# Performance work log

Measured on AMD Instinct MI355X. Metric: run time of the kernel, lower is better.

The kernel has to match this reference:

```python
import jax, jax.numpy as jnp
import numpy as np

B, S, M, KD, VD, QD, H, NQ = 256, 200, 32, 128, 256, 128, 64, 10000
TA, TB, TC = 0.075, 0.088, 1.0  # triangular membership params a, b, c


def setup_inputs() -> dict:
    key = jax.random.key(0)
    ks = jax.random.split(key, 12)
    q_data = jax.random.randint(ks[0], (B, S), 0, NQ + 1)
    # kaiming-normal-ish embedding table; padding_idx=0 row zeroed
    q_embed_weight = jax.random.normal(ks[1], (NQ + 1, QD)) * np.sqrt(2.0 / QD)
    q_embed_weight = q_embed_weight.at[0].set(0.0)
    key_mem = jax.random.normal(ks[2], (M, KD)) * np.sqrt(2.0 / KD)
    value_mem = jax.random.normal(ks[3], (M, VD)) * np.sqrt(2.0 / VD)
    in_dim = VD + QD
    s = 1.0 / np.sqrt(H)
    W_ih = jax.random.uniform(ks[4], (4 * H, in_dim), minval=-s, maxval=s)
    W_hh = jax.random.uniform(ks[5], (4 * H, H), minval=-s, maxval=s)
    b_ih = jax.random.uniform(ks[6], (4 * H,), minval=-s, maxval=s)
    b_hh = jax.random.uniform(ks[7], (4 * H,), minval=-s, maxval=s)
    W_pred = jax.random.normal(ks[8], (1, H)) * np.sqrt(2.0 / H)
    b_pred = jnp.zeros((1,))
    init_h = jax.random.normal(ks[9], (B, H))
    init_c = jax.random.normal(ks[10], (B, H))
    return dict(q_data=q_data, q_embed_weight=q_embed_weight, key_mem=key_mem,
                value_mem=value_mem, W_ih=W_ih, W_hh=W_hh, b_ih=b_ih, b_hh=b_hh,
                W_pred=W_pred, b_pred=b_pred, init_h=init_h, init_c=init_c)


def triangular_layer(cw):
    """cw: [N, M] correlation weights -> [N] unique-row indices.
    Faithful to torch: trit-quantize each weight {0,1,2}, then map each row to its
    index in the (lexicographically sorted) unique-row table, which is exactly what
    the pairwise squared-distance matmul + (dist==0).nonzero() trick computes."""
    w = jnp.minimum((cw - TA) / (TB - TA), (TC - cw) / (TC - TB))
    w = jnp.maximum(w, 0.0)
    iv = jnp.where(w >= 0.6, 2, jnp.where(w >= 0.1, 1, 0)).astype(jnp.int32)  # [N, M]
    # pack 32 trits into two int32 keys (3^16 < 2^31)
    p = jnp.power(3, jnp.arange(16, dtype=jnp.int32))  # [16]
    kh = (iv[:, :16] * p).sum(1)
    kl = (iv[:, 16:] * p).sum(1)
    order = jnp.lexsort((kl, kh))  # primary key kh
    kh_s, kl_s = kh[order], kl[order]
    change = jnp.concatenate([jnp.zeros((1,), jnp.int32),
                              ((kh_s[1:] != kh_s[:-1]) | (kl_s[1:] != kl_s[:-1])).astype(jnp.int32)])
    rank_sorted = jnp.cumsum(change)
    inv = jnp.zeros(cw.shape[0], jnp.int32).at[order].set(rank_sorted)
    return inv


def reference(q_data, q_embed_weight, key_mem, value_mem, W_ih, W_hh, b_ih, b_hh,
              W_pred, b_pred, init_h, init_c):
    q_emb = q_embed_weight[q_data]                                  # [B,S,QD]
    cw = jax.nn.softmax(jnp.einsum('bsd,md->bsm', q_emb, key_mem))  # DKVMN attention
    read = jnp.einsum('bsm,mv->bsv', cw, value_mem)                 # [B,S,VD]
    ids = triangular_layer(cw.reshape(B * S, M))                    # [B*S]
    x = jnp.concatenate([read, q_emb], axis=-1)                     # [B,S,VD+QD]

    def step(carry, xt):
        h, c = carry
        g = xt @ W_ih.T + h @ W_hh.T + b_ih + b_hh
        i, f, gg, o = jnp.split(g, 4, axis=-1)
        c = jax.nn.sigmoid(f) * c + jax.nn.sigmoid(i) * jnp.tanh(gg)
        h = jax.nn.sigmoid(o) * jnp.tanh(c)
        return (h, c), h

    _, hs = jax.lax.scan(step, (init_h, init_c), jnp.swapaxes(x, 0, 1))
    hs = jnp.swapaxes(hs, 0, 1)                                     # [B,S,H]
    pred = jax.nn.sigmoid(hs @ W_pred.T + b_pred)[..., 0]           # [B,S]
    return pred, ids
```

## Files before the change

### kernel.cpp

```cpp
#include <hip/hip_runtime.h>

#define BB 256
#define SS 200
#define MM 32
#define KDIM 128
#define VDIM 256
#define QDIM 128
#define HH 64
#define NROWS 10001
#define NSAMP (BB*SS)
#define INDIM (VDIM+QDIM)
#define DHS 8192
#define DHMASK (DHS-1)
#define XR 16
#define NB_ATTN 1251

typedef unsigned long long u64;
typedef unsigned int u32;
typedef float f16v __attribute__((ext_vector_type(16)));

__device__ __forceinline__ float fexp(float x){ return __builtin_amdgcn_exp2f(x * 1.44269504f); }
__device__ __forceinline__ float fsigm(float x){ return __builtin_amdgcn_rcpf(1.f + fexp(-x)); }
__device__ __forceinline__ float ftanh(float x){ return 1.f - 2.f*__builtin_amdgcn_rcpf(1.f + fexp(2.f*x)); }
__device__ __forceinline__ int clampq(int q){ return q < 0 ? 0 : (q > NROWS-1 ? NROWS-1 : q); }

__device__ __forceinline__ u32 hash64(u64 x){
  x ^= x >> 33; x *= 0xff51afd7ed558ccdULL;
  x ^= x >> 33; x *= 0xc4ceb9fe1a85ec53ULL;
  x ^= x >> 33;
  return (u32)x;
}

__device__ __forceinline__ u64 shflx64(u64 v, int m){
  int lo = __shfl_xor((int)(u32)v, m, 64);
  int hi = __shfl_xor((int)(u32)(v >> 32), m, 64);
  return ((u64)(u32)hi << 32) | (u32)lo;
}

__global__ void k_tr(const float* __restrict__ W_ih, const float* __restrict__ key_mem,
                     float* __restrict__ WQT4, float* __restrict__ KT,
                     float* __restrict__ WVT, u32* __restrict__ present){
  int idx = blockIdx.x*256 + threadIdx.x;
  if (idx < 131072) {
    int dd = idx & 3, j = (idx >> 2) & 255, d4 = idx >> 10;
    WQT4[idx] = W_ih[j*INDIM + VDIM + 4*d4 + dd];
  } else if (idx < 135168) {
    int t = idx - 131072;
    int m = t & 31, d = t >> 5; KT[t] = key_mem[m*KDIM + d];
  } else if (idx < 200704) {
    int t = idx - 135168;
    int j = t & 255, v = t >> 8; WVT[v*256 + j] = W_ih[j*INDIM + v];
  } else {
    int t = idx - 200704;
    if (t < NROWS) present[t] = 0u;
  }
}

__global__ __launch_bounds__(256) void k_front(
    const float* __restrict__ emb, const float* __restrict__ KT,
    const float* __restrict__ val, const float* __restrict__ WVT,
    const int* __restrict__ q_data,
    float* __restrict__ CW, u64* __restrict__ KEYT,
    float* __restrict__ VW, u32* __restrict__ present){
  int bid = blockIdx.x;
  if (bid < NB_ATTN) {
    int w = threadIdx.x >> 6, l = threadIdx.x & 63;
    int half = l >> 5, m = l & 31;
    int row = 2*w + half;
    int n = bid*8 + row;
    __shared__ float se[8][QDIM];
    {
      int rA = bid*8 + 2*w, rB = rA + 1;
      if (rA < NROWS) { se[2*w  ][l] = emb[rA*QDIM + l]; se[2*w  ][l+64] = emb[rA*QDIM + l + 64]; }
      if (rB < NROWS) { se[2*w+1][l] = emb[rB*QDIM + l]; se[2*w+1][l+64] = emb[rB*QDIM + l + 64]; }
    }
    __syncthreads();
    bool valid = (n < NROWS);
    float logit = 0.f;
    if (valid)
      for (int d = 0; d < KDIM; ++d) logit += se[row][d] * KT[d*32 + m];
    float mx = logit;
    #pragma unroll
    for (int msk = 16; msk >= 1; msk >>= 1) mx = fmaxf(mx, __shfl_xor(mx, msk, 64));
    float e = valid ? expf(logit - mx) : 0.f;
    float sum = e;
    #pragma unroll
    for (int msk = 16; msk >= 1; msk >>= 1) sum += __shfl_xor(sum, msk, 64);
    float cw = e / sum;
    float wv = fminf((cw - 0.075f)/0.013f, (1.0f - cw)/0.912f);
    wv = fmaxf(wv, 0.f);
    int iv = (wv >= 0.6f) ? 2 : ((wv >= 0.1f) ? 1 : 0);
    int ee = (m < 16) ? m + 16 : m - 16;
    u64 p3 = 1, bb = 3;
    #pragma unroll
    for (int bit = 0; bit < 5; ++bit) {
      if (ee & (1 << bit)) p3 *= bb;
      bb *= bb;
    }
    u64 term = valid ? (u64)iv * p3 : 0ULL;
    #pragma unroll
    for (int msk = 16; msk >= 1; msk >>= 1) term += shflx64(term, msk);
    if (valid) CW[n*256 + m] = cw;
    if (valid && m == 0) KEYT[n] = term;
  } else if (bid < NB_ATTN + MM) {
    int m = bid - NB_ATTN, j = threadIdx.x;
    __shared__ float sval[VDIM];
    sval[j] = val[m*VDIM + j];
    __syncthreads();
    float a0=0.f, a1=0.f, a2=0.f, a3=0.f;
    for (int v = 0; v < VDIM; v += 4) {
      a0 += sval[v+0]*WVT[(v+0)*256 + j];
      a1 += sval[v+1]*WVT[(v+1)*256 + j];
      a2 += sval[v+2]*WVT[(v+2)*256 + j];
      a3 += sval[v+3]*WVT[(v+3)*256 + j];
    }
    VW[m*256 + j] = (a0+a1)+(a2+a3);
  } else {
    int i = (bid - NB_ATTN - MM)*256 + threadIdx.x;
    if (i < NSAMP) present[clampq(q_data[i])] = 1u;
  }
}

__global__ __launch_bounds__(256) void k_xw(
    const float* __restrict__ CW, const float* __restrict__ emb,
    const float* __restrict__ VW, const float* __restrict__ WQT4,
    const float* __restrict__ b_ih, const float* __restrict__ b_hh,
    float* __restrict__ XW4){
  int base = blockIdx.x * XR;
  int j = threadIdx.x;
  __shared__ float scw[XR][32];
  __shared__ __align__(16) float ses[XR][QDIM];
  for (int idx = j; idx < XR*32; idx += 256) {
    int r = idx >> 5, m = idx & 31, n = base + r;
    scw[r][m] = (n < NROWS) ? CW[n*256 + m] : 0.f;
  }
  for (int idx = j; idx < XR*QDIM; idx += 256) {
    int r = idx >> 7, d = idx & 127, n = base + r;
    ses[r][d] = (n < NROWS) ? emb[n*QDIM + d] : 0.f;
  }
  __syncthreads();
  float bias = b_ih[j] + b_hh[j];
  float acc[XR];
  #pragma unroll
  for (int r = 0; r < XR; ++r) acc[r] = bias;
  for (int m = 0; m < MM; ++m) {
    float wv = VW[m*256 + j];
    #pragma unroll
    for (int r = 0; r < XR; ++r) acc[r] += scw[r][m] * wv;
  }
  for (int d4 = 0; d4 < QDIM/4; ++d4) {
    float4 wq = *(const float4*)(WQT4 + d4*1024 + j*4);
    #pragma unroll
    for (int r = 0; r < XR; ++r) {
      float4 ev = *(const float4*)(&ses[r][4*d4]);
      acc[r] += ev.x*wq.x + ev.y*wq.y + ev.z*wq.z + ev.w*wq.w;
    }
  }
  int gate = j >> 6, unit = j & 63;
  #pragma unroll
  for (int r = 0; r < XR; ++r)
    if (base + r < NROWS) XW4[(size_t)(base + r)*256 + 4*unit + gate] = acc[r];
}

__global__ __launch_bounds__(1024) void k_dedup(
    const u32* __restrict__ present, const u64* __restrict__ KEYT,
    u32* __restrict__ g_htab, u32* __restrict__ g_pay,
    u32* __restrict__ counter, u64* __restrict__ uniq){
  __shared__ u32 sh_tab[DHS];
  __shared__ u32 sh_pay[DHS];
  __shared__ u32 sh_cnt;
  int tid = threadIdx.x;
  for (int i = tid; i < DHS; i += 1024) sh_tab[i] = 0u;
  if (tid == 0) sh_cnt = 0u;
  __syncthreads();
  for (int n = tid; n < NROWS; n += 1024) {
    if (present[n] != 1u) continue;
    u64 key = KEYT[n];
    u32 h = hash64(key) & DHMASK;
    while (true) {
      u32 cur = sh_tab[h];
      if (cur != 0u) {
        if (KEYT[cur-1u] == key) break;
        h = (h + 1) & DHMASK; continue;
      }
      u32 prev = atomicCAS(&sh_tab[h], 0u, (u32)(n + 1));
      if (prev == 0u) {
        u32 idx = atomicAdd(&sh_cnt, 1u);
        uniq[idx] = key;
        sh_pay[h] = idx;
        break;
      }
      if (KEYT[prev-1u] == key) break;
      h = (h + 1) & DHMASK;
    }
  }
  __syncthreads();
  for (int i = tid; i < DHS; i += 1024) {
    u32 v = sh_tab[i];
    g_htab[i] = v;
    g_pay[i]  = v ? sh_pay[i] : 0u;
  }
  if (tid == 0) *counter = sh_cnt;
}

__global__ __launch_bounds__(64) void k_rank(const u64* __restrict__ uniq,
                                             const u32* __restrict__ counter,
                                             u32* __restrict__ RANK){
  u32 U = *counter;
  int u = blockIdx.x*64 + threadIdx.x;
  if (u >= (int)U) return;
  u64 mykey = uniq[u];
  u32 cnt = 0;
  for (u32 j = 0; j < U; ++j) {
    u64 k = uniq[j];
    cnt += (k < mykey) ? 1u : 0u;
  }
  RANK[u] = cnt;
}

__global__ void k_qrank(const u32* __restrict__ present, const u64* __restrict__ KEYT,
                        const u32* __restrict__ g_htab, const u32* __restrict__ g_pay,
                        const u32* __restrict__ RANK, u32* __restrict__ RANKQ){
  int n = blockIdx.x*blockDim.x + threadIdx.x;
  if (n >= NROWS || present[n] != 1u) return;
  u64 key = KEYT[n];
  u32 h = hash64(key) & DHMASK;
  while (true) {
    u32 cur = g_htab[h];
    if (cur != 0u && KEYT[cur-1u] == key) { RANKQ[n] = RANK[g_pay[h]]; return; }
    h = (h + 1) & DHMASK;
  }
}

__global__ void k_ids(const int* __restrict__ q_data, const u32* __restrict__ RANKQ,
                      float* __restrict__ out_ids){
  int i = blockIdx.x*blockDim.x + threadIdx.x;
  if (i >= NSAMP) return;
  out_ids[i] = (float)RANKQ[clampq(q_data[i])];
}

#define DOT16(acc, W, H) do { \
  acc += (W)[0]*(H)[0];   acc += (W)[1]*(H)[1];   acc += (W)[2]*(H)[2];   acc += (W)[3]*(H)[3]; \
  acc += (W)[4]*(H)[4];   acc += (W)[5]*(H)[5];   acc += (W)[6]*(H)[6];   acc += (W)[7]*(H)[7]; \
  acc += (W)[8]*(H)[8];   acc += (W)[9]*(H)[9];   acc += (W)[10]*(H)[10]; acc += (W)[11]*(H)[11]; \
  acc += (W)[12]*(H)[12]; acc += (W)[13]*(H)[13]; acc += (W)[14]*(H)[14]; acc += (W)[15]*(H)[15]; \
} while(0)

__global__ __launch_bounds__(256, 1) void k_lstm(
    const int* __restrict__ q_data, const float* __restrict__ XW4,
    const float* __restrict__ W_hh,
    const float* __restrict__ W_pred, const float* __restrict__ b_pred,
    const float* __restrict__ init_h, const float* __restrict__ init_c,
    float* __restrict__ out_pred){
  const int b = blockIdx.x;
  const int t = threadIdx.x;
  const int w = t >> 6, l = t & 63;
  const int uo = l & 15, k = l >> 4;
  const int u = 16*w + uo;
  __shared__ __align__(64) float Hbuf[SS][64];
  __shared__ int   sq[SS];
  __shared__ float swp[HH];

  for (int s = t; s < SS; s += 256) sq[s] = clampq(q_data[b*SS + s]);
  if (t < HH) swp[t] = W_pred[t];

  const float* wb = W_hh + (size_t)u*HH + 16*k;
  f16v Wi = *(const f16v*)(wb +     0);
  f16v Wf = *(const f16v*)(wb +  4096);
  f16v Wg = *(const f16v*)(wb +  8192);
  f16v Wo = *(const f16v*)(wb + 12288);

  f16v H = *(const f16v*)(init_h + (size_t)b*HH + 16*k);
  float c  = init_c[b*HH + u];
  float bp = b_pred[0];
  __syncthreads();

  float4 xwA = *(const float4*)(XW4 + (size_t)sq[0]*256 + 4*u);
  float4 xwB = *(const float4*)(XW4 + (size_t)sq[1]*256 + 4*u);

  for (int s = 0; s < SS; ++s) {
    int sp = (s + 2 < SS) ? s + 2 : SS - 1;
    float4 xwC = *(const float4*)(XW4 + (size_t)sq[sp]*256 + 4*u);
    float pi=0.f, pf=0.f, pg=0.f, po=0.f;
    DOT16(pi, Wi, H); DOT16(pf, Wf, H); DOT16(pg, Wg, H); DOT16(po, Wo, H);
    pi += __shfl_xor(pi, 16, 64); pf += __shfl_xor(pf, 16, 64);
    pg += __shfl_xor(pg, 16, 64); po += __shfl_xor(po, 16, 64);
    pi += __shfl_xor(pi, 32, 64); pf += __shfl_xor(pf, 32, 64);
    pg += __shfl_xor(pg, 32, 64); po += __shfl_xor(po, 32, 64);
    float ai = xwA.x + pi;
    float af = xwA.y + pf;
    float ag = xwA.z + pg;
    float ao = xwA.w + po;
    c = fsigm(af)*c + fsigm(ai)*ftanh(ag);
    float hh = fsigm(ao)*ftanh(c);
    if (l < 16) Hbuf[s][u] = hh;
    __syncthreads();
    H = *(const f16v*)(&Hbuf[s][16*k]);
    xwA = xwB; xwB = xwC;
  }
  __syncthreads();

  for (int s = t; s < SS; s += 256) {
    float acc = 0.f;
    #pragma unroll 16
    for (int kk = 0; kk < HH; ++kk) {
      int k2 = (kk + t) & 63;
      acc += Hbuf[s][k2] * swp[k2];
    }
    out_pred[b*SS + s] = fsigm(acc + bp);
  }
}

extern "C" void kernel_launch(void* const* d_in, const int* in_sizes, int n_in,
                              void* d_out, int out_size, void* d_ws, size_t ws_size,
                              hipStream_t stream) {
  const int*   q_data  = (const int*)d_in[0];
  const float* emb     = (const float*)d_in[1];
  const float* keym    = (const float*)d_in[2];
  const float* val     = (const float*)d_in[3];
  const float* W_ih    = (const float*)d_in[4];
  const float* W_hh    = (const float*)d_in[5];
  const float* b_ih    = (const float*)d_in[6];
  const float* b_hh    = (const float*)d_in[7];
  const float* W_pred  = (const float*)d_in[8];
  const float* b_pred  = (const float*)d_in[9];
  const float* init_h  = (const float*)d_in[10];
  const float* init_c  = (const float*)d_in[11];

  char* ws = (char*)d_ws;
  float* XW4     = (float*)(ws + 0);
  float* VW      = (float*)(ws + 10241024);
  u64*  KEYT     = (u64*) (ws + 10273792);
  u64*  uniq     = (u64*) (ws + 10353920);
  u32*  RANK     = (u32*) (ws + 10434048);
  u32*  g_htab   = (u32*) (ws + 10474240);
  u32*  g_pay    = (u32*) (ws + 10507008);
  u32*  counter  = (u32*) (ws + 10539776);
  u32*  present  = (u32*) (ws + 10539840);
  u32*  RANKQ    = (u32*) (ws + 10579904);
  float* WQT4    = (float*)(ws + 10619968);
  float* KT      = (float*)(ws + 11144256);
  float* WVT     = (float*)(ws + 11160640);
  float* CW      = XW4;

  float* out_pred = (float*)d_out;
  float* out_ids  = out_pred + NSAMP;

  hipLaunchKernelGGL(k_tr,    dim3(824), dim3(256), 0, stream,
                     W_ih, keym, WQT4, KT, WVT, present);
  hipLaunchKernelGGL(k_front, dim3(NB_ATTN + MM + 200), dim3(256), 0, stream,
                     emb, KT, val, WVT, q_data, CW, KEYT, VW, present);
  hipLaunchKernelGGL(k_dedup, dim3(1), dim3(1024), 0, stream,
                     present, KEYT, g_htab, g_pay, counter, uniq);
  hipLaunchKernelGGL(k_rank,  dim3((NROWS+63)/64), dim3(64), 0, stream, uniq, counter, RANK);
  hipLaunchKernelGGL(k_qrank, dim3((NROWS+255)/256), dim3(256), 0, stream,
                     present, KEYT, g_htab, g_pay, RANK, RANKQ);
  hipLaunchKernelGGL(k_xw,    dim3((NROWS+XR-1)/XR), dim3(256), 0, stream,
                     CW, emb, VW, WQT4, b_ih, b_hh, XW4);
  hipLaunchKernelGGL(k_ids,   dim3((NSAMP+255)/256), dim3(256), 0, stream, q_data, RANKQ, out_ids);
  hipLaunchKernelGGL(k_lstm,  dim3(BB), dim3(256), 0, stream,
                     q_data, XW4, W_hh, W_pred, b_pred, init_h, init_c, out_pred);
}
```

Before: 234.0 us.

## Drop transpose and ids kernels, fold work into front, dedup and LSTM

Removes the separate transpose kernel by reading key_mem and W_ih rows directly with float4 loads in k_front, and moves the WQT4 transpose into extra k_front blocks. The presence array becomes a shared-memory bitmap built inside the single-block dedup kernel from q_data. The ids output is written in the LSTM epilogue instead of a separate kernel. This cuts two launches and a global clearing pass, but the dedup block now scans all 51200 samples serially on one CU, and the key_mem reads become strided per lane.

```diff
diff --git a/kernel.cpp b/kernel.cpp
--- a/kernel.cpp
+++ b/kernel.cpp
@@ -14,6 +14,9 @@
 #define DHMASK (DHS-1)
 #define XR 16
 #define NB_ATTN 1251
+#define NB_VW 32
+#define NB_WQ 512
+#define NBM 320
 
 typedef unsigned long long u64;
 typedef unsigned int u32;
@@ -37,38 +40,18 @@
   return ((u64)(u32)hi << 32) | (u32)lo;
 }
 
-__global__ void k_tr(const float* __restrict__ W_ih, const float* __restrict__ key_mem,
-                     float* __restrict__ WQT4, float* __restrict__ KT,
-                     float* __restrict__ WVT, u32* __restrict__ present){
-  int idx = blockIdx.x*256 + threadIdx.x;
-  if (idx < 131072) {
-    int dd = idx & 3, j = (idx >> 2) & 255, d4 = idx >> 10;
-    WQT4[idx] = W_ih[j*INDIM + VDIM + 4*d4 + dd];
-  } else if (idx < 135168) {
-    int t = idx - 131072;
-    int m = t & 31, d = t >> 5; KT[t] = key_mem[m*KDIM + d];
-  } else if (idx < 200704) {
-    int t = idx - 135168;
-    int j = t & 255, v = t >> 8; WVT[v*256 + j] = W_ih[j*INDIM + v];
-  } else {
-    int t = idx - 200704;
-    if (t < NROWS) present[t] = 0u;
-  }
-}
-
 __global__ __launch_bounds__(256) void k_front(
-    const float* __restrict__ emb, const float* __restrict__ KT,
-    const float* __restrict__ val, const float* __restrict__ WVT,
-    const int* __restrict__ q_data,
+    const float* __restrict__ emb, const float* __restrict__ keym,
+    const float* __restrict__ val, const float* __restrict__ W_ih,
     float* __restrict__ CW, u64* __restrict__ KEYT,
-    float* __restrict__ VW, u32* __restrict__ present){
+    float* __restrict__ VW, float* __restrict__ WQT4){
   int bid = blockIdx.x;
   if (bid < NB_ATTN) {
     int w = threadIdx.x >> 6, l = threadIdx.x & 63;
     int half = l >> 5, m = l & 31;
     int row = 2*w + half;
     int n = bid*8 + row;
-    __shared__ float se[8][QDIM];
+    __shared__ __align__(16) float se[8][QDIM];
     {
       int rA = bid*8 + 2*w, rB = rA + 1;
       if (rA < NROWS) { se[2*w  ][l] = emb[rA*QDIM + l]; se[2*w  ][l+64] = emb[rA*QDIM + l + 64]; }
@@ -77,8 +60,17 @@
     __syncthreads();
     bool valid = (n < NROWS);
     float logit = 0.f;
-    if (valid)
-      for (int d = 0; d < KDIM; ++d) logit += se[row][d] * KT[d*32 + m];
+    if (valid) {
+      const float4* km = (const float4*)(keym + (size_t)m*KDIM);
+      for (int dq = 0; dq < KDIM/4; ++dq) {
+        float4 k4 = km[dq];
+        float4 e4 = *(const float4*)(&se[row][4*dq]);
+        logit += e4.x*k4.x;
+        logit += e4.y*k4.y;
+        logit += e4.z*k4.z;
+        logit += e4.w*k4.w;
+      }
+    }
     float mx = logit;
     #pragma unroll
     for (int msk = 16; msk >= 1; msk >>= 1) mx = fmaxf(mx, __shfl_xor(mx, msk, 64));
@@ -102,22 +94,25 @@
     for (int msk = 16; msk >= 1; msk >>= 1) term += shflx64(term, msk);
     if (valid) CW[n*256 + m] = cw;
     if (valid && m == 0) KEYT[n] = term;
-  } else if (bid < NB_ATTN + MM) {
+  } else if (bid < NB_ATTN + NB_VW) {
     int m = bid - NB_ATTN, j = threadIdx.x;
-    __shared__ float sval[VDIM];
+    __shared__ __align__(16) float sval[VDIM];
     sval[j] = val[m*VDIM + j];
     __syncthreads();
+    const float4* wr = (const float4*)(W_ih + (size_t)j*INDIM);
     float a0=0.f, a1=0.f, a2=0.f, a3=0.f;
-    for (int v = 0; v < VDIM; v += 4) {
-      a0 += sval[v+0]*WVT[(v+0)*256 + j];
-      a1 += sval[v+1]*WVT[(v+1)*256 + j];
-      a2 += sval[v+2]*WVT[(v+2)*256 + j];
-      a3 += sval[v+3]*WVT[(v+3)*256 + j];
+    for (int v4 = 0; v4 < VDIM/4; ++v4) {
+      float4 w4 = wr[v4];
+      a0 += sval[4*v4+0]*w4.x;
+      a1 += sval[4*v4+1]*w4.y;
+      a2 += sval[4*v4+2]*w4.z;
+      a3 += sval[4*v4+3]*w4.w;
     }
     VW[m*256 + j] = (a0+a1)+(a2+a3);
   } else {
-    int i = (bid - NB_ATTN - MM)*256 + threadIdx.x;
-    if (i < NSAMP) present[clampq(q_data[i])] = 1u;
+    int idx = (bid - NB_ATTN - NB_VW)*256 + threadIdx.x;
+    int dd = idx & 3, j = (idx >> 2) & 255, d4 = idx >> 10;
+    WQT4[idx] = W_ih[j*INDIM + VDIM + 4*d4 + dd];
   }
 }
 
@@ -163,18 +158,26 @@
 }
 
 __global__ __launch_bounds__(1024) void k_dedup(
-    const u32* __restrict__ present, const u64* __restrict__ KEYT,
+    const int* __restrict__ q_data, const u64* __restrict__ KEYT,
     u32* __restrict__ g_htab, u32* __restrict__ g_pay,
-    u32* __restrict__ counter, u64* __restrict__ uniq){
+    u32* __restrict__ counter, u64* __restrict__ uniq,
+    u32* __restrict__ presentw){
   __shared__ u32 sh_tab[DHS];
   __shared__ u32 sh_pay[DHS];
+  __shared__ u32 sh_bm[NBM];
   __shared__ u32 sh_cnt;
   int tid = threadIdx.x;
   for (int i = tid; i < DHS; i += 1024) sh_tab[i] = 0u;
+  if (tid < NBM) sh_bm[tid] = 0u;
   if (tid == 0) sh_cnt = 0u;
   __syncthreads();
+  for (int i = tid; i < NSAMP; i += 1024) {
+    int q = clampq(q_data[i]);
+    atomicOr(&sh_bm[q >> 5], 1u << (q & 31));
+  }
+  __syncthreads();
   for (int n = tid; n < NROWS; n += 1024) {
-    if (present[n] != 1u) continue;
+    if (!((sh_bm[n >> 5] >> (n & 31)) & 1u)) continue;
     u64 key = KEYT[n];
     u32 h = hash64(key) & DHMASK;
     while (true) {
@@ -200,6 +203,7 @@
     g_htab[i] = v;
     g_pay[i]  = v ? sh_pay[i] : 0u;
   }
+  if (tid < NBM) presentw[tid] = sh_bm[tid];
   if (tid == 0) *counter = sh_cnt;
 }
 
@@ -218,11 +222,12 @@
   RANK[u] = cnt;
 }
 
-__global__ void k_qrank(const u32* __restrict__ present, const u64* __restrict__ KEYT,
+__global__ void k_qrank(const u32* __restrict__ presentw, const u64* __restrict__ KEYT,
                         const u32* __restrict__ g_htab, const u32* __restrict__ g_pay,
                         const u32* __restrict__ RANK, u32* __restrict__ RANKQ){
   int n = blockIdx.x*blockDim.x + threadIdx.x;
-  if (n >= NROWS || present[n] != 1u) return;
+  if (n >= NROWS) return;
+  if (!((presentw[n >> 5] >> (n & 31)) & 1u)) return;
   u64 key = KEYT[n];
   u32 h = hash64(key) & DHMASK;
   while (true) {
@@ -232,13 +237,6 @@
   }
 }
 
-__global__ void k_ids(const int* __restrict__ q_data, const u32* __restrict__ RANKQ,
-                      float* __restrict__ out_ids){
-  int i = blockIdx.x*blockDim.x + threadIdx.x;
-  if (i >= NSAMP) return;
-  out_ids[i] = (float)RANKQ[clampq(q_data[i])];
-}
-
 #define DOT16(acc, W, H) do { \
   acc += (W)[0]*(H)[0];   acc += (W)[1]*(H)[1];   acc += (W)[2]*(H)[2];   acc += (W)[3]*(H)[3]; \
   acc += (W)[4]*(H)[4];   acc += (W)[5]*(H)[5];   acc += (W)[6]*(H)[6];   acc += (W)[7]*(H)[7]; \
@@ -251,7 +249,8 @@
     const float* __restrict__ W_hh,
     const float* __restrict__ W_pred, const float* __restrict__ b_pred,
     const float* __restrict__ init_h, const float* __restrict__ init_c,
-    float* __restrict__ out_pred){
+    const u32* __restrict__ RANKQ,
+    float* __restrict__ out_pred, float* __restrict__ out_ids){
   const int b = blockIdx.x;
   const int t = threadIdx.x;
   const int w = t >> 6, l = t & 63;
@@ -308,6 +307,7 @@
       acc += Hbuf[s][k2] * swp[k2];
     }
     out_pred[b*SS + s] = fsigm(acc + bp);
+    out_ids[b*SS + s]  = (float)RANKQ[sq[s]];
   }
 }
 
@@ -336,28 +336,24 @@
   u32*  g_htab   = (u32*) (ws + 10474240);
   u32*  g_pay    = (u32*) (ws + 10507008);
   u32*  counter  = (u32*) (ws + 10539776);
-  u32*  present  = (u32*) (ws + 10539840);
+  u32*  presentw = (u32*) (ws + 10539840);
   u32*  RANKQ    = (u32*) (ws + 10579904);
   float* WQT4    = (float*)(ws + 10619968);
-  float* KT      = (float*)(ws + 11144256);
-  float* WVT     = (float*)(ws + 11160640);
   float* CW      = XW4;
 
   float* out_pred = (float*)d_out;
   float* out_ids  = out_pred + NSAMP;
 
-  hipLaunchKernelGGL(k_tr,    dim3(824), dim3(256), 0, stream,
-                     W_ih, keym, WQT4, KT, WVT, present);
-  hipLaunchKernelGGL(k_front, dim3(NB_ATTN + MM + 200), dim3(256), 0, stream,
-                     emb, KT, val, WVT, q_data, CW, KEYT, VW, present);
+  hipLaunchKernelGGL(k_front, dim3(NB_ATTN + NB_VW + NB_WQ), dim3(256), 0, stream,
+                     emb, keym, val, W_ih, CW, KEYT, VW, WQT4);
   hipLaunchKernelGGL(k_dedup, dim3(1), dim3(1024), 0, stream,
-                     present, KEYT, g_htab, g_pay, counter, uniq);
+                     q_data, KEYT, g_htab, g_pay, counter, uniq, presentw);
   hipLaunchKernelGGL(k_rank,  dim3((NROWS+63)/64), dim3(64), 0, stream, uniq, counter, RANK);
   hipLaunchKernelGGL(k_qrank, dim3((NROWS+255)/256), dim3(256), 0, stream,
-                     present, KEYT, g_htab, g_pay, RANK, RANKQ);
+                     presentw, KEYT, g_htab, g_pay, RANK, RANKQ);
   hipLaunchKernelGGL(k_xw,    dim3((NROWS+XR-1)/XR), dim3(256), 0, stream,
                      CW, emb, VW, WQT4, b_ih, b_hh, XW4);
-  hipLaunchKernelGGL(k_ids,   dim3((NSAMP+255)/256), dim3(256), 0, stream, q_data, RANKQ, out_ids);
   hipLaunchKernelGGL(k_lstm,  dim3(BB), dim3(256), 0, stream,
-                     q_data, XW4, W_hh, W_pred, b_pred, init_h, init_c, out_pred);
-}
+                     q_data, XW4, W_hh, W_pred, b_pred, init_h, init_c,
+                     RANKQ, out_pred, out_ids);
+}
```

After: 259.6 us. +10.9%, slower.
